# Performance work log

Measured on AMD Instinct MI355X. Metric: run time of the kernel, lower is better.

## Reference

```python
import jax, jax.numpy as jnp
import numpy as np

D_MODEL = 2048
NUM_HEADS = 16
D_K = D_MODEL // NUM_HEADS
BASE = 10000.0


def rotate_half(x):
    half = x.shape[-1] // 2
    x1, x2 = x[..., :half], x[..., half:]
    return jnp.concatenate((-x2, x1), axis=-1)


def setup_inputs() -> dict:
    key = jax.random.key(0)
    ks = jax.random.split(key, 9)
    B, S = 2, 2048
    std = 1.0 / np.sqrt(D_MODEL)
    inp = {"x": jax.random.normal(ks[0], (B, S, D_MODEL), dtype=jnp.float32)}
    for i, name in enumerate(["q", "k", "v", "o"]):
        inp[f"w_{name}"] = jax.random.uniform(ks[1 + i], (D_MODEL, D_MODEL), jnp.float32, -std, std)
        inp[f"b_{name}"] = jax.random.uniform(ks[5 + i], (D_MODEL,), jnp.float32, -std, std)
    return inp


def reference(x, w_q, b_q, w_k, b_k, w_v, b_v, w_o, b_o):
    B, S, _ = x.shape
    # projections -> (B, H, S, d_k)
    def proj(w, b):
        y = x @ w.T + b
        return y.reshape(B, S, NUM_HEADS, D_K).transpose(0, 2, 1, 3)
    Q, K, V = proj(w_q, b_q), proj(w_k, b_k), proj(w_v, b_v)
    # rotary embeddings
    inv_freq = 1.0 / (BASE ** (jnp.arange(0, D_K, 2, dtype=jnp.float32) / D_K))
    t = jnp.arange(S, dtype=jnp.float32)
    freqs = jnp.einsum("i,j->ij", t, inv_freq)  # (S, d_k/2)
    emb = jnp.concatenate((freqs, freqs), axis=-1)  # (S, d_k)
    cos, sin = jnp.cos(emb), jnp.sin(emb)
    Q = Q * cos + rotate_half(Q) * sin
    K = K * cos + rotate_half(K) * sin
    # attention
    scores = jnp.einsum("bhqd,bhkd->bhqk", Q, K) / np.sqrt(D_K).astype(np.float32)
    attn = jax.nn.softmax(scores, axis=-1)  # dropout p=0 (eval)
    out = jnp.einsum("bhqk,bhkd->bhqd", attn, V)
    out = out.transpose(0, 2, 1, 3).reshape(B, S, D_MODEL)
    return out @ w_o.T + b_o
```

## Files before the change

kernel.cpp:

```cpp
#include <hip/hip_runtime.h>
#include <hip/hip_bf16.h>
#include <math.h>


#define D_MODEL 2048
#define NHEADS  16
#define DK      128
#define BATCH   2
#define SEQ     2048
#define MTOT    (BATCH*SEQ)
#define XN      (MTOT*D_MODEL)
#define WN      (D_MODEL*D_MODEL)

typedef __attribute__((ext_vector_type(8))) short bf16x8;
typedef __attribute__((ext_vector_type(4))) float f32x4;
typedef __attribute__((ext_vector_type(8))) unsigned short u16x8;

__device__ __forceinline__ float bf2f(unsigned short u) {
    union { unsigned int i; float f; } v; v.i = ((unsigned int)u) << 16; return v.f;
}
__device__ __forceinline__ unsigned short f2bfu(float f) {
    __hip_bfloat16 h = __float2bfloat16(f);
    return *reinterpret_cast<unsigned short*>(&h);
}
__device__ __forceinline__ void async_copy16(const unsigned short* g, unsigned short* l) {
    __builtin_amdgcn_global_load_lds((const __attribute__((address_space(1))) void*)g,
                                     (__attribute__((address_space(3))) void*)l, 16, 0, 0);
}

__global__ void rope_table_kernel(float2* __restrict__ cs) {
    int idx = blockIdx.x * blockDim.x + threadIdx.x;
    if (idx >= SEQ * 64) return;
    int s = idx >> 6, j = idx & 63;
    double inv = pow(10000.0, -(double)j / 64.0);
    double f = (double)s * inv;
    cs[idx] = make_float2((float)cos(f), (float)sin(f));
}

__global__ void convert_kernel(const float* __restrict__ x,
                               const float* __restrict__ wq, const float* __restrict__ wk,
                               const float* __restrict__ wv, const float* __restrict__ wo,
                               unsigned short* __restrict__ Xbf, unsigned short* __restrict__ Wbf) {
    size_t e = ((size_t)blockIdx.x * blockDim.x + threadIdx.x) * 4;
    const float* src; unsigned short* dst;
    if (e < XN) { src = x + e; dst = Xbf + e; }
    else {
        size_t r = e - XN; int w = (int)(r >> 22); size_t o = r & (WN - 1);
        src = (w == 0 ? wq : w == 1 ? wk : w == 2 ? wv : wo) + o;
        dst = Wbf + (size_t)w * WN + o;
    }
    float4 v = *(const float4*)src;
    ushort4 u;
    u.x = f2bfu(v.x); u.y = f2bfu(v.y); u.z = f2bfu(v.z); u.w = f2bfu(v.w);
    *(ushort4*)dst = u;
}

#define BM 128
#define BN 128
#define BK 32

template<int AMODE, int CMODE>
__global__ __launch_bounds__(256, 2)
void gemm_bf16_kernel(const unsigned short* __restrict__ A,
                      const unsigned short* __restrict__ W,
                      const float* __restrict__ bias, void* __restrict__ Cout) {
    __shared__ unsigned short smem[8704];
    const int tid = threadIdx.x;
    const int lane = tid & 63, wid = tid >> 6;
    const int wm = wid >> 1, wn = wid & 1;
    const int m0 = blockIdx.x * BM, n0 = blockIdx.y * BN;

    f32x4 acc[4][4];
    #pragma unroll
    for (int i = 0; i < 4; ++i)
        #pragma unroll
        for (int j = 0; j < 4; ++j) acc[i][j] = (f32x4){0.f, 0.f, 0.f, 0.f};

    const int lrow = lane & 15, lkc = lane >> 4;

    for (int k0 = 0; k0 < D_MODEL; k0 += BK) {
        #pragma unroll
        for (int i = 0; i < 4; ++i) {
            const int off = i * 4096 + wid * 1024 + lane * 16;
            const unsigned short* src;
            if (i < 2) {
                int elem = off >> 1, row = elem >> 5, col = elem & 31;
                if (AMODE == 0) {
                    src = A + (size_t)(m0 + row) * D_MODEL + k0 + col;
                } else {
                    int m = m0 + row, b = m >> 11, s = m & 2047;
                    src = A + (((size_t)(b * NHEADS + (k0 >> 7))) * SEQ + s) * DK + (k0 & 127) + col;
                }
            } else {
                int elem = (off - 8192) >> 1, row = elem >> 5, col = elem & 31;
                src = W + (size_t)(n0 + row) * D_MODEL + k0 + col;
            }
            async_copy16(src, &smem[(i * 4096 + wid * 1024) >> 1]);
        }
        __syncthreads();

        bf16x8 a[4], b[4];
        #pragma unroll
        for (int mi = 0; mi < 4; ++mi)
            a[mi] = *(const bf16x8*)&smem[(wm * 64 + mi * 16 + lrow) * 32 + lkc * 8];
        #pragma unroll
        for (int ni = 0; ni < 4; ++ni)
            b[ni] = *(const bf16x8*)&smem[4096 + (wn * 64 + ni * 16 + lrow) * 32 + lkc * 8];
        #pragma unroll
        for (int mi = 0; mi < 4; ++mi)
            #pragma unroll
            for (int ni = 0; ni < 4; ++ni)
                acc[mi][ni] = __builtin_amdgcn_mfma_f32_16x16x32_bf16(a[mi], b[ni], acc[mi][ni], 0, 0, 0);
        __syncthreads();
    }

    const int lq = lane >> 4;
    if (CMODE != 2) {
        #pragma unroll
        for (int ni = 0; ni < 4; ++ni) {
            int col = n0 + wn * 64 + ni * 16 + lrow;
            float bv = bias[col];
            #pragma unroll
            for (int mi = 0; mi < 4; ++mi) {
                #pragma unroll
                for (int r = 0; r < 4; ++r) {
                    int row = m0 + wm * 64 + mi * 16 + lq * 4 + r;
                    float v = acc[mi][ni][r] + bv;
                    if (CMODE == 0) {
                        ((float*)Cout)[(size_t)row * D_MODEL + col] = v;
                    } else {
                        int bb = row >> 11, s = row & 2047, h = col >> 7, d = col & 127;
                        ((unsigned short*)Cout)[(((size_t)(bb * NHEADS + h)) * SEQ + s) * DK + d] = f2bfu(v);
                    }
                }
            }
        }
    } else {
        const int b = m0 >> 11;
        const int h = n0 >> 7;
        const int sbase = m0 & 2047;
        unsigned short* vtbase = (unsigned short*)Cout +
            (((size_t)(b * NHEADS + h)) * DK) * SEQ + sbase;
        #pragma unroll
        for (int half = 0; half < 2; ++half) {
            __syncthreads();
            if (wn == half) {
                #pragma unroll
                for (int ni = 0; ni < 4; ++ni) {
                    float bv = bias[n0 + half * 64 + ni * 16 + lrow];
                    #pragma unroll
                    for (int mi = 0; mi < 4; ++mi)
                        #pragma unroll
                        for (int r = 0; r < 4; ++r) {
                            int row = wm * 64 + mi * 16 + lq * 4 + r;
                            smem[row * 68 + ni * 16 + lrow] = f2bfu(acc[mi][ni][r] + bv);
                        }
                }
            }
            __syncthreads();
            int dl = tid >> 2, s0 = (tid & 3) * 32;
            u16x8 o[4];
            #pragma unroll
            for (int j8 = 0; j8 < 4; ++j8)
                #pragma unroll
                for (int j = 0; j < 8; ++j)
                    o[j8][j] = smem[(s0 + j8 * 8 + j) * 68 + dl];
            unsigned short* dst = vtbase + (size_t)(half * 64 + dl) * SEQ + s0;
            #pragma unroll
            for (int j8 = 0; j8 < 4; ++j8)
                *(u16x8*)(dst + j8 * 8) = o[j8];
        }
    }
}

__global__ void rope_kernel(unsigned short* __restrict__ Q, unsigned short* __restrict__ Kt,
                            const float2* __restrict__ cs) {
    const float qscale = 0.08838834764831845f;
    int idx = blockIdx.x * blockDim.x + threadIdx.x;
    if (idx >= BATCH * NHEADS * SEQ * 8) return;
    int j8 = idx & 7, bhs = idx >> 3, s = bhs & (SEQ - 1);
    int d0 = j8 * 8;
    size_t base = (size_t)bhs * DK;
    u16x8 qlo = *(const u16x8*)(Q + base + d0);
    u16x8 qhi = *(const u16x8*)(Q + base + 64 + d0);
    u16x8 klo = *(const u16x8*)(Kt + base + d0);
    u16x8 khi = *(const u16x8*)(Kt + base + 64 + d0);
    u16x8 olo, ohi, plo, phi;
    #pragma unroll
    for (int j = 0; j < 8; ++j) {
        float2 c = cs[(s << 6) + d0 + j];
        float q0 = bf2f(qlo[j]), q1 = bf2f(qhi[j]);
        olo[j] = f2bfu((q0 * c.x - q1 * c.y) * qscale);
        ohi[j] = f2bfu((q1 * c.x + q0 * c.y) * qscale);
        float k0 = bf2f(klo[j]), k1 = bf2f(khi[j]);
        plo[j] = f2bfu(k0 * c.x - k1 * c.y);
        phi[j] = f2bfu(k1 * c.x + k0 * c.y);
    }
    *(u16x8*)(Q + base + d0) = olo;
    *(u16x8*)(Q + base + 64 + d0) = ohi;
    *(u16x8*)(Kt + base + d0) = plo;
    *(u16x8*)(Kt + base + 64 + d0) = phi;
}

#define AQT 64
#define AKT 64
#define NT  (SEQ/AKT)
#define PSS 72

__global__ __launch_bounds__(256, 2)
void attn_mfma_kernel(unsigned short* __restrict__ Q,
                      const unsigned short* __restrict__ Kp,
                      const unsigned short* __restrict__ VTp) {
    __shared__ unsigned short Ks[2][AKT * DK];
    __shared__ unsigned short Vs[2][DK * AKT];
    __shared__ unsigned short Ps[AQT * PSS];
    const int tid = threadIdx.x;
    const int lane = tid & 63, wid = tid >> 6;
    const int lrow = lane & 15, lkc = lane >> 4;
    const int bh = blockIdx.y;
    const int q0 = blockIdx.x * AQT;
    unsigned short* qpanel = Q + (size_t)bh * SEQ * DK;
    const unsigned short* kpanel  = Kp  + (size_t)bh * SEQ * DK;
    const unsigned short* vtpanel = VTp + (size_t)bh * DK * SEQ;

    bf16x8 qfrag[4];
    {
        const unsigned short* qsrc = qpanel + (size_t)(q0 + wid * 16 + lrow) * DK + lkc * 8;
        #pragma unroll
        for (int c = 0; c < 4; ++c)
            qfrag[c] = *(const bf16x8*)(qsrc + c * 32);
    }

    const int st_elem = wid * 512 + lane * 8;
    const int k_row = st_elem >> 7;
    const int k_colS = ((st_elem & 127)) ;
    const int v_d = st_elem >> 6;
    const int v_c = (st_elem >> 3) & 7;

#define STAGE(tt, bb)                                                                   \
    {                                                                                   \
        int kv0 = (tt) * AKT;                                                           \
        _Pragma("unroll")                                                               \
        for (int i = 0; i < 4; ++i) {                                                   \
            int row = i * 16 + k_row;                                                   \
            int colS = k_colS ^ ((row & 7) << 3);                                       \
            async_copy16(kpanel + (size_t)(kv0 + row) * DK + colS,                      \
                         &Ks[bb][i * 2048 + wid * 512]);                                \
        }                                                                               \
        _Pragma("unroll")                                                               \
        for (int i = 0; i < 4; ++i) {                                                   \
            int d = i * 32 + v_d;                                                       \
            int cS = v_c ^ (d & 7);                                                     \
            async_copy16(vtpanel + (size_t)d * SEQ + kv0 + cS * 8,                      \
                         &Vs[bb][i * 2048 + wid * 512]);                                \
        }                                                                               \
    }

    float m_i[4], l_i[4];
    f32x4 oacc[8];
    #pragma unroll
    for (int r = 0; r < 4; ++r) { m_i[r] = -1e30f; l_i[r] = 0.f; }
    #pragma unroll
    for (int dt = 0; dt < 8; ++dt) oacc[dt] = (f32x4){0.f, 0.f, 0.f, 0.f};

    STAGE(0, 0);
    int buf = 0;

    for (int tt = 0; tt < NT; ++tt) {
        if (tt + 1 < NT) {
            STAGE(tt + 1, buf ^ 1);
            asm volatile("s_waitcnt vmcnt(8)" ::: "memory");
        } else {
            asm volatile("s_waitcnt vmcnt(0)" ::: "memory");
        }
        __builtin_amdgcn_sched_barrier(0);
        __builtin_amdgcn_s_barrier();

        const unsigned short* KsB = Ks[buf];
        const unsigned short* VsB = Vs[buf];

        f32x4 sacc[4];
        #pragma unroll
        for (int t = 0; t < 4; ++t) sacc[t] = (f32x4){0.f, 0.f, 0.f, 0.f};
        #pragma unroll
        for (int t = 0; t < 4; ++t) {
            int krl = t * 16 + lrow;
            int sw = (krl & 7) << 3;
            #pragma unroll
            for (int c = 0; c < 4; ++c) {
                bf16x8 kf = *(const bf16x8*)&KsB[(krl * DK + c * 32 + lkc * 8) ^ sw];
                sacc[t] = __builtin_amdgcn_mfma_f32_16x16x32_bf16(qfrag[c], kf, sacc[t], 0, 0, 0);
            }
        }

        float mx[4];
        #pragma unroll
        for (int r = 0; r < 4; ++r) {
            float v = fmaxf(fmaxf(sacc[0][r], sacc[1][r]), fmaxf(sacc[2][r], sacc[3][r]));
            #pragma unroll
            for (int off = 1; off <= 8; off <<= 1)
                v = fmaxf(v, __shfl_xor(v, off, 64));
            mx[r] = v;
        }
        int cond = (mx[0] - m_i[0] <= 8.f) && (mx[1] - m_i[1] <= 8.f) &&
                   (mx[2] - m_i[2] <= 8.f) && (mx[3] - m_i[3] <= 8.f);
        if (!__all(cond)) {
            #pragma unroll
            for (int r = 0; r < 4; ++r) {
                float mnew = fmaxf(m_i[r], mx[r]);
                float corr = __expf(m_i[r] - mnew);
                l_i[r] *= corr;
                #pragma unroll
                for (int dt = 0; dt < 8; ++dt) oacc[dt][r] *= corr;
                m_i[r] = mnew;
            }
        }
        #pragma unroll
        for (int r = 0; r < 4; ++r) {
            float p0 = __expf(sacc[0][r] - m_i[r]);
            float p1 = __expf(sacc[1][r] - m_i[r]);
            float p2 = __expf(sacc[2][r] - m_i[r]);
            float p3 = __expf(sacc[3][r] - m_i[r]);
            float rs = (p0 + p1) + (p2 + p3);
            #pragma unroll
            for (int off = 1; off <= 8; off <<= 1)
                rs += __shfl_xor(rs, off, 64);
            l_i[r] += rs;
            int pb = (wid * 16 + lkc * 4 + r) * PSS;
            Ps[pb + lrow]      = f2bfu(p0);
            Ps[pb + 16 + lrow] = f2bfu(p1);
            Ps[pb + 32 + lrow] = f2bfu(p2);
            Ps[pb + 48 + lrow] = f2bfu(p3);
        }

        const int arow = (wid * 16 + lrow) * PSS;
        bf16x8 pfA = *(const bf16x8*)&Ps[arow + lkc * 8];
        bf16x8 pfB = *(const bf16x8*)&Ps[arow + 32 + lkc * 8];
        #pragma unroll
        for (int dt = 0; dt < 8; ++dt) {
            int d = dt * 16 + lrow;
            int basev = d * 64;
            bf16x8 vfA = *(const bf16x8*)&VsB[basev + ((lkc     ^ (lrow & 7)) * 8)];
            bf16x8 vfB = *(const bf16x8*)&VsB[basev + (((lkc+4) ^ (lrow & 7)) * 8)];
            oacc[dt] = __builtin_amdgcn_mfma_f32_16x16x32_bf16(pfA, vfA, oacc[dt], 0, 0, 0);
            oacc[dt] = __builtin_amdgcn_mfma_f32_16x16x32_bf16(pfB, vfB, oacc[dt], 0, 0, 0);
        }

        asm volatile("s_waitcnt lgkmcnt(0)" ::: "memory");
        __builtin_amdgcn_sched_barrier(0);
        __builtin_amdgcn_s_barrier();
        buf ^= 1;
    }
#undef STAGE

    float inv[4];
    #pragma unroll
    for (int r = 0; r < 4; ++r) inv[r] = 1.0f / l_i[r];
    #pragma unroll
    for (int dt = 0; dt < 8; ++dt) {
        #pragma unroll
        for (int r = 0; r < 4; ++r) {
            int q = q0 + wid * 16 + lkc * 4 + r;
            qpanel[(size_t)q * DK + dt * 16 + lrow] = f2bfu(oacc[dt][r] * inv[r]);
        }
    }
}

extern "C" void kernel_launch(void* const* d_in, const int* in_sizes, int n_in,
                              void* d_out, int out_size, void* d_ws, size_t ws_size,
                              hipStream_t stream) {
    const float* x   = (const float*)d_in[0];
    const float* w_q = (const float*)d_in[1];
    const float* b_q = (const float*)d_in[2];
    const float* w_k = (const float*)d_in[3];
    const float* b_k = (const float*)d_in[4];
    const float* w_v = (const float*)d_in[5];
    const float* b_v = (const float*)d_in[6];
    const float* w_o = (const float*)d_in[7];
    const float* b_o = (const float*)d_in[8];
    float* out = (float*)d_out;

    char* ws = (char*)d_ws;
    const size_t bfTensor = (size_t)BATCH * NHEADS * SEQ * DK * 2;
    unsigned short* Qbf  = (unsigned short*)(ws);
    unsigned short* Kbf  = (unsigned short*)(ws + bfTensor);
    unsigned short* VTbf = (unsigned short*)(ws + 2 * bfTensor);
    unsigned short* Xbf  = (unsigned short*)(ws + 3 * bfTensor);
    unsigned short* Wbf  = (unsigned short*)(ws + 4 * bfTensor);
    float2*         cs   = (float2*)(ws + 6 * bfTensor);

    rope_table_kernel<<<(SEQ * 64 + 255) / 256, 256, 0, stream>>>(cs);
    convert_kernel<<<(XN + 4 * WN) / 4 / 256, 256, 0, stream>>>(x, w_q, w_k, w_v, w_o, Xbf, Wbf);

    dim3 ggrid(MTOT / BM, D_MODEL / BN);
    gemm_bf16_kernel<0, 1><<<ggrid, 256, 0, stream>>>(Xbf, Wbf + 0 * (size_t)WN, b_q, Qbf);
    gemm_bf16_kernel<0, 1><<<ggrid, 256, 0, stream>>>(Xbf, Wbf + 1 * (size_t)WN, b_k, Kbf);
    gemm_bf16_kernel<0, 2><<<ggrid, 256, 0, stream>>>(Xbf, Wbf + 2 * (size_t)WN, b_v, VTbf);

    rope_kernel<<<(BATCH * NHEADS * SEQ * 8 + 255) / 256, 256, 0, stream>>>(Qbf, Kbf, cs);

    attn_mfma_kernel<<<dim3(SEQ / AQT, BATCH * NHEADS), 256, 0, stream>>>(Qbf, Kbf, VTbf);

    gemm_bf16_kernel<1, 0><<<ggrid, 256, 0, stream>>>(Qbf, Wbf + 3 * (size_t)WN, b_o, out);
}
```

Baseline: 508.5 us.

## Process two 16-row query fragments per wave in attention to reuse K/V tiles

The attention query tile grows from 64 to 128 rows, so each wave now owns 32 query rows as two 16-row MFMA fragments. Each K fragment and V fragment read from LDS feeds two MFMAs instead of one, which halves K/V global staging and LDS traffic per query row. The single P staging buffer is reused in turn for the two fragments. It also raises wave priority around the MFMA sections with s_setprio. The cost is roughly double the accumulator registers and half as many blocks in the grid, which may lower occupancy and load balance.

```diff
diff --git a/kernel.cpp b/kernel.cpp
--- a/kernel.cpp
+++ b/kernel.cpp
@@ -202,7 +202,7 @@
     *(u16x8*)(Kt + base + 64 + d0) = phi;
 }
 
-#define AQT 64
+#define AQT 128
 #define AKT 64
 #define NT  (SEQ/AKT)
 #define PSS 72
@@ -213,7 +213,7 @@
                       const unsigned short* __restrict__ VTp) {
     __shared__ unsigned short Ks[2][AKT * DK];
     __shared__ unsigned short Vs[2][DK * AKT];
-    __shared__ unsigned short Ps[AQT * PSS];
+    __shared__ unsigned short Ps[64 * PSS];
     const int tid = threadIdx.x;
     const int lane = tid & 63, wid = tid >> 6;
     const int lrow = lane & 15, lkc = lane >> 4;
@@ -223,17 +223,19 @@
     const unsigned short* kpanel  = Kp  + (size_t)bh * SEQ * DK;
     const unsigned short* vtpanel = VTp + (size_t)bh * DK * SEQ;
 
-    bf16x8 qfrag[4];
-    {
-        const unsigned short* qsrc = qpanel + (size_t)(q0 + wid * 16 + lrow) * DK + lkc * 8;
+    bf16x8 qfrag[2][4];
+    #pragma unroll
+    for (int f = 0; f < 2; ++f) {
+        const unsigned short* qsrc =
+            qpanel + (size_t)(q0 + wid * 32 + f * 16 + lrow) * DK + lkc * 8;
         #pragma unroll
         for (int c = 0; c < 4; ++c)
-            qfrag[c] = *(const bf16x8*)(qsrc + c * 32);
+            qfrag[f][c] = *(const bf16x8*)(qsrc + c * 32);
     }
 
     const int st_elem = wid * 512 + lane * 8;
     const int k_row = st_elem >> 7;
-    const int k_colS = ((st_elem & 127)) ;
+    const int k_colS = (st_elem & 127);
     const int v_d = st_elem >> 6;
     const int v_c = (st_elem >> 3) & 7;
 
@@ -256,12 +258,15 @@
         }                                                                               \
     }
 
-    float m_i[4], l_i[4];
-    f32x4 oacc[8];
+    float m_i[2][4], l_i[2][4];
+    f32x4 oacc[2][8];
     #pragma unroll
-    for (int r = 0; r < 4; ++r) { m_i[r] = -1e30f; l_i[r] = 0.f; }
-    #pragma unroll
-    for (int dt = 0; dt < 8; ++dt) oacc[dt] = (f32x4){0.f, 0.f, 0.f, 0.f};
+    for (int f = 0; f < 2; ++f) {
+        #pragma unroll
+        for (int r = 0; r < 4; ++r) { m_i[f][r] = -1e30f; l_i[f][r] = 0.f; }
+        #pragma unroll
+        for (int dt = 0; dt < 8; ++dt) oacc[f][dt] = (f32x4){0.f, 0.f, 0.f, 0.f};
+    }
 
     STAGE(0, 0);
     int buf = 0;
@@ -279,9 +284,12 @@
         const unsigned short* KsB = Ks[buf];
         const unsigned short* VsB = Vs[buf];
 
-        f32x4 sacc[4];
-        #pragma unroll
-        for (int t = 0; t < 4; ++t) sacc[t] = (f32x4){0.f, 0.f, 0.f, 0.f};
+        f32x4 sacc[2][4];
+        #pragma unroll
+        for (int f = 0; f < 2; ++f)
+            #pragma unroll
+            for (int t = 0; t < 4; ++t) sacc[f][t] = (f32x4){0.f, 0.f, 0.f, 0.f};
+        __builtin_amdgcn_s_setprio(1);
         #pragma unroll
         for (int t = 0; t < 4; ++t) {
             int krl = t * 16 + lrow;
@@ -289,62 +297,73 @@
             #pragma unroll
             for (int c = 0; c < 4; ++c) {
                 bf16x8 kf = *(const bf16x8*)&KsB[(krl * DK + c * 32 + lkc * 8) ^ sw];
-                sacc[t] = __builtin_amdgcn_mfma_f32_16x16x32_bf16(qfrag[c], kf, sacc[t], 0, 0, 0);
-            }
-        }
-
-        float mx[4];
-        #pragma unroll
-        for (int r = 0; r < 4; ++r) {
-            float v = fmaxf(fmaxf(sacc[0][r], sacc[1][r]), fmaxf(sacc[2][r], sacc[3][r]));
-            #pragma unroll
-            for (int off = 1; off <= 8; off <<= 1)
-                v = fmaxf(v, __shfl_xor(v, off, 64));
-            mx[r] = v;
-        }
-        int cond = (mx[0] - m_i[0] <= 8.f) && (mx[1] - m_i[1] <= 8.f) &&
-                   (mx[2] - m_i[2] <= 8.f) && (mx[3] - m_i[3] <= 8.f);
-        if (!__all(cond)) {
+                sacc[0][t] = __builtin_amdgcn_mfma_f32_16x16x32_bf16(qfrag[0][c], kf, sacc[0][t], 0, 0, 0);
+                sacc[1][t] = __builtin_amdgcn_mfma_f32_16x16x32_bf16(qfrag[1][c], kf, sacc[1][t], 0, 0, 0);
+            }
+        }
+        __builtin_amdgcn_s_setprio(0);
+
+        bf16x8 pf[2][2];
+        #pragma unroll
+        for (int f = 0; f < 2; ++f) {
+            float mx[4];
             #pragma unroll
             for (int r = 0; r < 4; ++r) {
-                float mnew = fmaxf(m_i[r], mx[r]);
-                float corr = __expf(m_i[r] - mnew);
-                l_i[r] *= corr;
-                #pragma unroll
-                for (int dt = 0; dt < 8; ++dt) oacc[dt][r] *= corr;
-                m_i[r] = mnew;
-            }
-        }
-        #pragma unroll
-        for (int r = 0; r < 4; ++r) {
-            float p0 = __expf(sacc[0][r] - m_i[r]);
-            float p1 = __expf(sacc[1][r] - m_i[r]);
-            float p2 = __expf(sacc[2][r] - m_i[r]);
-            float p3 = __expf(sacc[3][r] - m_i[r]);
-            float rs = (p0 + p1) + (p2 + p3);
-            #pragma unroll
-            for (int off = 1; off <= 8; off <<= 1)
-                rs += __shfl_xor(rs, off, 64);
-            l_i[r] += rs;
-            int pb = (wid * 16 + lkc * 4 + r) * PSS;
-            Ps[pb + lrow]      = f2bfu(p0);
-            Ps[pb + 16 + lrow] = f2bfu(p1);
-            Ps[pb + 32 + lrow] = f2bfu(p2);
-            Ps[pb + 48 + lrow] = f2bfu(p3);
-        }
-
-        const int arow = (wid * 16 + lrow) * PSS;
-        bf16x8 pfA = *(const bf16x8*)&Ps[arow + lkc * 8];
-        bf16x8 pfB = *(const bf16x8*)&Ps[arow + 32 + lkc * 8];
+                float v = fmaxf(fmaxf(sacc[f][0][r], sacc[f][1][r]),
+                                fmaxf(sacc[f][2][r], sacc[f][3][r]));
+                #pragma unroll
+                for (int off = 1; off <= 8; off <<= 1)
+                    v = fmaxf(v, __shfl_xor(v, off, 64));
+                mx[r] = v;
+            }
+            int cond = (mx[0] - m_i[f][0] <= 8.f) && (mx[1] - m_i[f][1] <= 8.f) &&
+                       (mx[2] - m_i[f][2] <= 8.f) && (mx[3] - m_i[f][3] <= 8.f);
+            if (!__all(cond)) {
+                #pragma unroll
+                for (int r = 0; r < 4; ++r) {
+                    float mnew = fmaxf(m_i[f][r], mx[r]);
+                    float corr = __expf(m_i[f][r] - mnew);
+                    l_i[f][r] *= corr;
+                    #pragma unroll
+                    for (int dt = 0; dt < 8; ++dt) oacc[f][dt][r] *= corr;
+                    m_i[f][r] = mnew;
+                }
+            }
+            #pragma unroll
+            for (int r = 0; r < 4; ++r) {
+                float p0 = __expf(sacc[f][0][r] - m_i[f][r]);
+                float p1 = __expf(sacc[f][1][r] - m_i[f][r]);
+                float p2 = __expf(sacc[f][2][r] - m_i[f][r]);
+                float p3 = __expf(sacc[f][3][r] - m_i[f][r]);
+                float rs = (p0 + p1) + (p2 + p3);
+                #pragma unroll
+                for (int off = 1; off <= 8; off <<= 1)
+                    rs += __shfl_xor(rs, off, 64);
+                l_i[f][r] += rs;
+                int pb = (wid * 16 + lkc * 4 + r) * PSS;
+                Ps[pb + lrow]      = f2bfu(p0);
+                Ps[pb + 16 + lrow] = f2bfu(p1);
+                Ps[pb + 32 + lrow] = f2bfu(p2);
+                Ps[pb + 48 + lrow] = f2bfu(p3);
+            }
+            const int arow = (wid * 16 + lrow) * PSS;
+            pf[f][0] = *(const bf16x8*)&Ps[arow + lkc * 8];
+            pf[f][1] = *(const bf16x8*)&Ps[arow + 32 + lkc * 8];
+        }
+
+        __builtin_amdgcn_s_setprio(1);
         #pragma unroll
         for (int dt = 0; dt < 8; ++dt) {
             int d = dt * 16 + lrow;
             int basev = d * 64;
             bf16x8 vfA = *(const bf16x8*)&VsB[basev + ((lkc     ^ (lrow & 7)) * 8)];
             bf16x8 vfB = *(const bf16x8*)&VsB[basev + (((lkc+4) ^ (lrow & 7)) * 8)];
-            oacc[dt] = __builtin_amdgcn_mfma_f32_16x16x32_bf16(pfA, vfA, oacc[dt], 0, 0, 0);
-            oacc[dt] = __builtin_amdgcn_mfma_f32_16x16x32_bf16(pfB, vfB, oacc[dt], 0, 0, 0);
-        }
+            oacc[0][dt] = __builtin_amdgcn_mfma_f32_16x16x32_bf16(pf[0][0], vfA, oacc[0][dt], 0, 0, 0);
+            oacc[0][dt] = __builtin_amdgcn_mfma_f32_16x16x32_bf16(pf[0][1], vfB, oacc[0][dt], 0, 0, 0);
+            oacc[1][dt] = __builtin_amdgcn_mfma_f32_16x16x32_bf16(pf[1][0], vfA, oacc[1][dt], 0, 0, 0);
+            oacc[1][dt] = __builtin_amdgcn_mfma_f32_16x16x32_bf16(pf[1][1], vfB, oacc[1][dt], 0, 0, 0);
+        }
+        __builtin_amdgcn_s_setprio(0);
 
         asm volatile("s_waitcnt lgkmcnt(0)" ::: "memory");
         __builtin_amdgcn_sched_barrier(0);
@@ -353,15 +372,18 @@
     }
 #undef STAGE
 
-    float inv[4];
     #pragma unroll
-    for (int r = 0; r < 4; ++r) inv[r] = 1.0f / l_i[r];
-    #pragma unroll
-    for (int dt = 0; dt < 8; ++dt) {
-        #pragma unroll
-        for (int r = 0; r < 4; ++r) {
-            int q = q0 + wid * 16 + lkc * 4 + r;
-            qpanel[(size_t)q * DK + dt * 16 + lrow] = f2bfu(oacc[dt][r] * inv[r]);
+    for (int f = 0; f < 2; ++f) {
+        float inv[4];
+        #pragma unroll
+        for (int r = 0; r < 4; ++r) inv[r] = 1.0f / l_i[f][r];
+        #pragma unroll
+        for (int dt = 0; dt < 8; ++dt) {
+            #pragma unroll
+            for (int r = 0; r < 4; ++r) {
+                int q = q0 + wid * 32 + f * 16 + lkc * 4 + r;
+                qpanel[(size_t)q * DK + dt * 16 + lrow] = f2bfu(oacc[f][dt][r] * inv[r]);
+            }
         }
     }
 }
```

Result: faster. 477.6 us (-6.1%).
